# Kernel optimization log

Hardware: AMD Instinct MI355X
Metric: run time of the kernel (lower is better)

Reference implementation:

```python
import jax, jax.numpy as jnp
import numpy as np

N, D, NUM_CLASSES = 8192, 256, 64
MARGIN_SAME = 0.9
MARGIN_DIFF = 0.5


def setup_inputs() -> dict:
    key = jax.random.key(0)
    k1, k2 = jax.random.split(key)
    inputs = jax.random.normal(k1, (N, D), dtype=jnp.float32)
    # contrastive losses with cosine-style margins expect unit-norm embeddings
    inputs = inputs / jnp.linalg.norm(inputs, axis=1, keepdims=True)
    targets = jax.random.randint(k2, (N,), 0, NUM_CLASSES, dtype=jnp.int64)
    return {"inputs": inputs, "targets": targets}


def reference(inputs, targets):
    n = inputs.shape[0]
    sim = jnp.matmul(inputs, inputs.T)  # [n, n] pairwise similarities

    same = targets[:, None] == targets[None, :]  # [n, n]
    pos_mask = same & (sim < 1.0)                # pos_pair_ selection per row
    neg_mask = ~same                             # neg_pair_ selection per row

    pos_active = pos_mask & (sim < MARGIN_SAME)  # contribute 1 - sim
    neg_active = neg_mask & (sim > MARGIN_DIFF)  # contribute sim

    # sum over all rows, divided by n (sort in the original is irrelevant to sums)
    loss = (jnp.sum(jnp.where(pos_active, 1.0 - sim, 0.0))
            + jnp.sum(jnp.where(neg_active, sim, 0.0))) / n

    prec = jnp.float32(0.0)  # original: c is never incremented

    # original reports means of the LAST row's pos_pair_ / neg_pair_
    last_sim = sim[n - 1]
    lp = pos_mask[n - 1]
    ln = neg_mask[n - 1]
    mean_pos_sim = jnp.sum(jnp.where(lp, last_sim, 0.0)) / jnp.maximum(
        jnp.sum(lp).astype(jnp.float32), 1.0)
    mean_neg_sim = jnp.sum(jnp.where(ln, last_sim, 0.0)) / jnp.maximum(
        jnp.sum(ln).astype(jnp.float32), 1.0)

    return (loss, prec, mean_pos_sim, mean_neg_sim)
```

## Files before the change

### kernel.cpp

```cpp
#include <hip/hip_runtime.h>
#include <hip/hip_bf16.h>

#define N_ 8192
#define D_ 256
#define BM 128
#define NB (N_ / BM)
#define NT (NB * (NB + 1) / 2)

typedef float f32x4 __attribute__((ext_vector_type(4)));


__global__ void prep_kernel(const float* __restrict__ X, const int* __restrict__ tg,
                            unsigned char* __restrict__ Xb, double* __restrict__ accd) {
  if (blockIdx.x < 512) {
    if (blockIdx.x == 0 && threadIdx.x < 96) accd[threadIdx.x] = 0.0;
    int t = blockIdx.x * 256 + threadIdx.x;
    int r = t >> 4, pc = t & 15;
    int w = pc >> 2, s = pc & 3;
    const float* row = X + (size_t)r * D_;
    int ka = w * 64 + s * 8;
    float4 a0 = *(const float4*)(row + ka);
    float4 a1 = *(const float4*)(row + ka + 4);
    float4 b0 = *(const float4*)(row + ka + 32);
    float4 b1 = *(const float4*)(row + ka + 36);
    int4 d;
    d.x = __builtin_amdgcn_cvt_pk_fp8_f32(a0.x, a0.y, 0, false);
    d.x = __builtin_amdgcn_cvt_pk_fp8_f32(a0.z, a0.w, d.x, true);
    d.y = __builtin_amdgcn_cvt_pk_fp8_f32(a1.x, a1.y, 0, false);
    d.y = __builtin_amdgcn_cvt_pk_fp8_f32(a1.z, a1.w, d.y, true);
    d.z = __builtin_amdgcn_cvt_pk_fp8_f32(b0.x, b0.y, 0, false);
    d.z = __builtin_amdgcn_cvt_pk_fp8_f32(b0.z, b0.w, d.z, true);
    d.w = __builtin_amdgcn_cvt_pk_fp8_f32(b1.x, b1.y, 0, false);
    d.w = __builtin_amdgcn_cvt_pk_fp8_f32(b1.z, b1.w, d.w, true);
    *(int4*)(Xb + (size_t)r * 256 + pc * 16) = d;
  } else {
    int lb = blockIdx.x - 512;
    int lane = threadIdx.x & 63, wv = threadIdx.x >> 6;
    const float4* xl = (const float4*)(X + (size_t)(N_ - 1) * D_);
    float4 a = xl[lane];
    int tlast = tg[N_ - 1];
    double lp = 0, lpc = 0, ln = 0, lnc = 0;
    for (int cc = 0; cc < 16; ++cc) {
      int j = lb * 64 + wv * 16 + cc;
      float4 bq = ((const float4*)(X + (size_t)j * D_))[lane];
      double s = (double)a.x * bq.x + (double)a.y * bq.y +
                 (double)a.z * bq.z + (double)a.w * bq.w;
#pragma unroll
      for (int off = 32; off; off >>= 1) s += __shfl_down(s, off);
      if (lane == 0) {
        float sf = (float)s;
        bool same = (tg[j] == tlast);
        if (same && sf < 1.0f) { lp += sf; lpc += 1.0; }
        if (!same) { ln += sf; lnc += 1.0; }
      }
    }
    if (lane == 0) {
      double* slot = accd + 128 + (size_t)(lb * 4 + wv) * 4;
      slot[0] = lp; slot[1] = lpc; slot[2] = ln; slot[3] = lnc;
    }
  }
}

__global__ __launch_bounds__(256, 4) void simloss_kernel(
    const unsigned char* __restrict__ Xb, const int* __restrict__ tg,
    double* __restrict__ accd) {
  __shared__ __align__(16) char lds[2 * 16384];
  __shared__ float red[12];

  const int t0 = blockIdx.x;
  const int t = (t0 & 7) * (NT / 8) + (t0 >> 3);

  int bi = (int)(((2.0f * NB + 1.0f) -
                  sqrtf((2.0f * NB + 1.0f) * (2.0f * NB + 1.0f) - 8.0f * (float)t)) * 0.5f);
  if (bi < 0) bi = 0;
  if (bi > NB - 1) bi = NB - 1;
  while (((bi + 1) * NB - ((bi + 1) * bi) / 2) <= t) ++bi;
  while ((bi * NB - (bi * (bi - 1)) / 2) > t) --bi;
  const int bj = bi + (t - (bi * NB - (bi * (bi - 1)) / 2));

  const int tid = threadIdx.x;
  const int lane = tid & 63, wv = tid >> 6;
  const int wr = wv >> 1, wc = wv & 1;
  const int rowA0 = bi * BM, rowB0 = bj * BM;

  const int srow = tid >> 2;
  const int sw = (tid & 3) ^ ((srow >> 1) & 3);
  const unsigned char* bA = Xb + (size_t)(rowA0 + srow) * 256 + sw * 16;
  const unsigned char* bB = Xb + (size_t)(rowB0 + srow) * 256 + sw * 16;

#define GLDS(g, l) \
  __builtin_amdgcn_global_load_lds((const __attribute__((address_space(1))) void*)(g), \
                                   (__attribute__((address_space(3))) void*)(l), 16, 0, 0)
#define STAGE(buf, kt)                                       \
  do {                                                       \
    char* base = lds + (buf) * 16384;                        \
    GLDS(bA + (kt) * 64, base + tid * 16);                   \
    GLDS(bA + 16384 + (kt) * 64, base + 4096 + tid * 16);    \
    GLDS(bB + (kt) * 64, base + 8192 + tid * 16);            \
    GLDS(bB + 16384 + (kt) * 64, base + 12288 + tid * 16);   \
  } while (0)

  const int fr = lane & 15, slv = lane >> 4;
  const int rswz = slv ^ ((fr >> 1) & 3);
  const int aoff = (wr * 64 + fr) * 64 + rswz * 16;
  const int boff = 8192 + (wc * 64 + fr) * 64 + rswz * 16;

  f32x4 acc[4][4] = {};
  union U { int4 v; long l[2]; };

  STAGE(0, 0);
  STAGE(1, 1);

#pragma unroll
  for (int kt = 0; kt < 4; ++kt) {
    if (kt < 3)
      asm volatile("s_waitcnt vmcnt(4)" ::: "memory");
    else
      asm volatile("s_waitcnt vmcnt(0)" ::: "memory");
    __builtin_amdgcn_s_barrier();

    const char* Ab = lds + (kt & 1) * 16384;
    U a[4], b[4];
#pragma unroll
    for (int m = 0; m < 4; ++m) a[m].v = *(const int4*)(Ab + aoff + m * 1024);
#pragma unroll
    for (int n = 0; n < 4; ++n) b[n].v = *(const int4*)(Ab + boff + n * 1024);
#pragma unroll
    for (int m = 0; m < 4; ++m)
#pragma unroll
      for (int n = 0; n < 4; ++n) {
        acc[m][n] = __builtin_amdgcn_mfma_f32_16x16x32_fp8_fp8(a[m].l[0], b[n].l[0],
                                                               acc[m][n], 0, 0, 0);
        acc[m][n] = __builtin_amdgcn_mfma_f32_16x16x32_fp8_fp8(a[m].l[1], b[n].l[1],
                                                               acc[m][n], 0, 0, 0);
      }

    if (kt < 2) {
      asm volatile("s_waitcnt lgkmcnt(0)" ::: "memory");
      __builtin_amdgcn_sched_barrier(0);
      __builtin_amdgcn_s_barrier();
      STAGE(kt & 1, kt + 2);
    }
  }
#undef STAGE
#undef GLDS

  const int cRow = slv * 4, cCol = fr;
  int tj[4], ti[4][4];
#pragma unroll
  for (int n = 0; n < 4; ++n) tj[n] = tg[rowB0 + wc * 64 + n * 16 + cCol];
#pragma unroll
  for (int m = 0; m < 4; ++m)
#pragma unroll
    for (int r = 0; r < 4; ++r) ti[m][r] = tg[rowA0 + wr * 64 + m * 16 + cRow + r];

  float pc = 0.f, ps = 0.f, ns = 0.f;
#pragma unroll
  for (int m = 0; m < 4; ++m)
#pragma unroll
    for (int n = 0; n < 4; ++n)
#pragma unroll
      for (int r = 0; r < 4; ++r) {
        float s = acc[m][n][r];
        bool same = (ti[m][r] == tj[n]);
        if (same & (s < 0.9f)) { pc += 1.0f; ps += s; }
        if ((!same) & (s > 0.5f)) { ns += s; }
      }

#pragma unroll
  for (int off = 32; off > 0; off >>= 1) {
    pc += __shfl_down(pc, off);
    ps += __shfl_down(ps, off);
    ns += __shfl_down(ns, off);
  }
  if (lane == 0) { red[0 + wv] = pc; red[4 + wv] = ps; red[8 + wv] = ns; }
  __syncthreads();
  if (tid == 0) {
    double w = (bi == bj) ? 1.0 : 2.0;
    double* slot = accd + (blockIdx.x & 31) * 3;
    atomicAdd(&slot[0], w * (double)(red[0] + red[1] + red[2] + red[3]));
    atomicAdd(&slot[1], w * (double)(red[4] + red[5] + red[6] + red[7]));
    atomicAdd(&slot[2], w * (double)(red[8] + red[9] + red[10] + red[11]));
  }
}

__global__ void finalize_kernel(const double* __restrict__ accd, float* __restrict__ out) {
  int l = threadIdx.x;
  double lp = 0, lpc = 0, ln = 0, lnc = 0;
  for (int q = l; q < 512; q += 64) {
    const double* s = accd + 128 + (size_t)q * 4;
    lp += s[0]; lpc += s[1]; ln += s[2]; lnc += s[3];
  }
  double pc = 0, ps = 0, ns = 0;
  if (l < 32) { pc = accd[l * 3]; ps = accd[l * 3 + 1]; ns = accd[l * 3 + 2]; }
#pragma unroll
  for (int off = 32; off > 0; off >>= 1) {
    lp += __shfl_down(lp, off);  lpc += __shfl_down(lpc, off);
    ln += __shfl_down(ln, off);  lnc += __shfl_down(lnc, off);
    pc += __shfl_down(pc, off);  ps += __shfl_down(ps, off);
    ns += __shfl_down(ns, off);
  }
  if (l == 0) {
    out[0] = (float)((pc - ps + ns) / (double)N_);
    out[1] = 0.0f;
    out[2] = (float)(lp / fmax(lpc, 1.0));
    out[3] = (float)(ln / fmax(lnc, 1.0));
  }
}

extern "C" void kernel_launch(void* const* d_in, const int* in_sizes, int n_in,
                              void* d_out, int out_size, void* d_ws, size_t ws_size,
                              hipStream_t stream) {
  const float* X = (const float*)d_in[0];
  const int* tg = (const int*)d_in[1];
  float* out = (float*)d_out;
  double* accd = (double*)d_ws;
  unsigned char* Xb = (unsigned char*)d_ws + 32768;

  prep_kernel<<<512 + 128, 256, 0, stream>>>(X, tg, Xb, accd);
  simloss_kernel<<<NT, 256, 0, stream>>>(Xb, tg, accd);
  finalize_kernel<<<1, 64, 0, stream>>>(accd, out);
}
```

Measured before the change: 46.98 us.

## Process four column tiles per block reusing resident A tile in LDS

Each block now keeps its 128-row A tile resident in LDS for the full K depth and streams four consecutive B column tiles through a triple-buffered pipeline. Partial loss sums are reduced after each tile. The launch shrinks from 2080 single-tile blocks to 544 four-tile blocks, with padded tiles beyond the triangle given zero weight. This cuts redundant A loads and per-block overhead, but uses more LDS (launch bounds drop to 2) and wastes some work on padded tiles.

```diff
diff --git a/kernel.cpp b/kernel.cpp
--- a/kernel.cpp
+++ b/kernel.cpp
@@ -3,9 +3,7 @@
 
 #define N_ 8192
 #define D_ 256
-#define BM 128
-#define NB (N_ / BM)
-#define NT (NB * (NB + 1) / 2)
+#define NBLK 544
 
 typedef float f32x4 __attribute__((ext_vector_type(4)));
 
@@ -61,126 +59,158 @@
   }
 }
 
-__global__ __launch_bounds__(256, 4) void simloss_kernel(
+__global__ __launch_bounds__(256, 2) void simloss_kernel(
     const unsigned char* __restrict__ Xb, const int* __restrict__ tg,
     double* __restrict__ accd) {
-  __shared__ __align__(16) char lds[2 * 16384];
+  __shared__ __align__(16) char lds[32768 + 3 * 8192];
   __shared__ float red[12];
 
   const int t0 = blockIdx.x;
-  const int t = (t0 & 7) * (NT / 8) + (t0 >> 3);
-
-  int bi = (int)(((2.0f * NB + 1.0f) -
-                  sqrtf((2.0f * NB + 1.0f) * (2.0f * NB + 1.0f) - 8.0f * (float)t)) * 0.5f);
-  if (bi < 0) bi = 0;
-  if (bi > NB - 1) bi = NB - 1;
-  while (((bi + 1) * NB - ((bi + 1) * bi) / 2) <= t) ++bi;
-  while ((bi * NB - (bi * (bi - 1)) / 2) > t) --bi;
-  const int bj = bi + (t - (bi * NB - (bi * (bi - 1)) / 2));
+  const int b = (t0 & 7) * (NBLK / 8) + (t0 >> 3);
+#define FA(x) (66 * (x)-2 * (x) * (x))
+  int a = (int)((66.0f - sqrtf(4356.0f - 8.0f * (float)b)) * 0.25f);
+  if (a < 0) a = 0;
+  if (a > 15) a = 15;
+  while (a < 15 && FA(a + 1) <= b) ++a;
+  while (a > 0 && FA(a) > b) --a;
+  int off = b - FA(a);
+  const int nbb = 16 - a;
+  int r = 0;
+  while (off >= nbb) { off -= nbb; ++r; }
+  const int bi = 4 * a + r;
+  const int j0 = bi + 4 * off;
+#undef FA
 
   const int tid = threadIdx.x;
   const int lane = tid & 63, wv = tid >> 6;
   const int wr = wv >> 1, wc = wv & 1;
-  const int rowA0 = bi * BM, rowB0 = bj * BM;
+  const int rowA0 = bi * 128;
+
+  int bj[4];
+  float wt[4];
+#pragma unroll
+  for (int tt = 0; tt < 4; ++tt) {
+    int j = j0 + tt;
+    wt[tt] = (j > 63) ? 0.0f : (j == bi ? 1.0f : 2.0f);
+    bj[tt] = (j > 63) ? 63 : j;
+  }
+
+  const int fr = lane & 15, slv = lane >> 4;
+  const int cRow = slv * 4, cCol = fr;
+  int ti[4][4], tjq[4][4];
+#pragma unroll
+  for (int m = 0; m < 4; ++m) {
+    int4 v = *(const int4*)(tg + rowA0 + wr * 64 + m * 16 + cRow);
+    ti[m][0] = v.x; ti[m][1] = v.y; ti[m][2] = v.z; ti[m][3] = v.w;
+  }
+#pragma unroll
+  for (int tt = 0; tt < 4; ++tt)
+#pragma unroll
+    for (int n = 0; n < 4; ++n) tjq[tt][n] = tg[bj[tt] * 128 + wc * 64 + n * 16 + cCol];
 
   const int srow = tid >> 2;
   const int sw = (tid & 3) ^ ((srow >> 1) & 3);
   const unsigned char* bA = Xb + (size_t)(rowA0 + srow) * 256 + sw * 16;
-  const unsigned char* bB = Xb + (size_t)(rowB0 + srow) * 256 + sw * 16;
+  const unsigned char* pB[4];
+#pragma unroll
+  for (int tt = 0; tt < 4; ++tt)
+    pB[tt] = Xb + (size_t)(bj[tt] * 128 + srow) * 256 + sw * 16;
 
 #define GLDS(g, l) \
   __builtin_amdgcn_global_load_lds((const __attribute__((address_space(1))) void*)(g), \
                                    (__attribute__((address_space(3))) void*)(l), 16, 0, 0)
-#define STAGE(buf, kt)                                       \
-  do {                                                       \
-    char* base = lds + (buf) * 16384;                        \
-    GLDS(bA + (kt) * 64, base + tid * 16);                   \
-    GLDS(bA + 16384 + (kt) * 64, base + 4096 + tid * 16);    \
-    GLDS(bB + (kt) * 64, base + 8192 + tid * 16);            \
-    GLDS(bB + 16384 + (kt) * 64, base + 12288 + tid * 16);   \
+#define STAGE_B(s)                                              \
+  do {                                                          \
+    char* d = lds + 32768 + ((s) % 3) * 8192;                   \
+    const unsigned char* src = pB[(s) >> 2] + ((s)&3) * 64;     \
+    GLDS(src, d + tid * 16);                                    \
+    GLDS(src + 16384, d + 4096 + tid * 16);                     \
   } while (0)
 
-  const int fr = lane & 15, slv = lane >> 4;
+  __builtin_amdgcn_sched_barrier(0);
+#pragma unroll
+  for (int kt = 0; kt < 4; ++kt) {
+    GLDS(bA + kt * 64, lds + kt * 8192 + tid * 16);
+    GLDS(bA + 16384 + kt * 64, lds + kt * 8192 + 4096 + tid * 16);
+  }
+  STAGE_B(0);
+  STAGE_B(1);
+
   const int rswz = slv ^ ((fr >> 1) & 3);
   const int aoff = (wr * 64 + fr) * 64 + rswz * 16;
-  const int boff = 8192 + (wc * 64 + fr) * 64 + rswz * 16;
+  const int boff = (wc * 64 + fr) * 64 + rswz * 16;
 
   f32x4 acc[4][4] = {};
+  float pcT = 0.f, psT = 0.f, nsT = 0.f;
   union U { int4 v; long l[2]; };
 
-  STAGE(0, 0);
-  STAGE(1, 1);
-
-#pragma unroll
-  for (int kt = 0; kt < 4; ++kt) {
-    if (kt < 3)
-      asm volatile("s_waitcnt vmcnt(4)" ::: "memory");
+#pragma unroll
+  for (int s = 0; s < 16; ++s) {
+    asm volatile("s_waitcnt lgkmcnt(0)" ::: "memory");
+    __builtin_amdgcn_sched_barrier(0);
+    if (s < 15)
+      asm volatile("s_waitcnt vmcnt(2)" ::: "memory");
     else
       asm volatile("s_waitcnt vmcnt(0)" ::: "memory");
     __builtin_amdgcn_s_barrier();
-
-    const char* Ab = lds + (kt & 1) * 16384;
-    U a[4], b[4];
-#pragma unroll
-    for (int m = 0; m < 4; ++m) a[m].v = *(const int4*)(Ab + aoff + m * 1024);
-#pragma unroll
-    for (int n = 0; n < 4; ++n) b[n].v = *(const int4*)(Ab + boff + n * 1024);
+    if (s + 2 < 16) STAGE_B(s + 2);
+
+    const int kt = s & 3, tt = s >> 2;
+    const char* Ab = lds + kt * 8192;
+    const char* Bb = lds + 32768 + (s % 3) * 8192;
+    U a4[4], b4[4];
+#pragma unroll
+    for (int m = 0; m < 4; ++m) a4[m].v = *(const int4*)(Ab + aoff + m * 1024);
+#pragma unroll
+    for (int n = 0; n < 4; ++n) b4[n].v = *(const int4*)(Bb + boff + n * 1024);
 #pragma unroll
     for (int m = 0; m < 4; ++m)
 #pragma unroll
       for (int n = 0; n < 4; ++n) {
-        acc[m][n] = __builtin_amdgcn_mfma_f32_16x16x32_fp8_fp8(a[m].l[0], b[n].l[0],
+        acc[m][n] = __builtin_amdgcn_mfma_f32_16x16x32_fp8_fp8(a4[m].l[0], b4[n].l[0],
                                                                acc[m][n], 0, 0, 0);
-        acc[m][n] = __builtin_amdgcn_mfma_f32_16x16x32_fp8_fp8(a[m].l[1], b[n].l[1],
+        acc[m][n] = __builtin_amdgcn_mfma_f32_16x16x32_fp8_fp8(a4[m].l[1], b4[n].l[1],
                                                                acc[m][n], 0, 0, 0);
       }
 
-    if (kt < 2) {
-      asm volatile("s_waitcnt lgkmcnt(0)" ::: "memory");
-      __builtin_amdgcn_sched_barrier(0);
-      __builtin_amdgcn_s_barrier();
-      STAGE(kt & 1, kt + 2);
+    if (kt == 3) {
+      float pc = 0.f, ps = 0.f, ns = 0.f;
+#pragma unroll
+      for (int m = 0; m < 4; ++m)
+#pragma unroll
+        for (int n = 0; n < 4; ++n)
+#pragma unroll
+          for (int rg = 0; rg < 4; ++rg) {
+            float sv = acc[m][n][rg];
+            bool same = (ti[m][rg] == tjq[tt][n]);
+            if (same & (sv < 0.9f)) { pc += 1.0f; ps += sv; }
+            if ((!same) & (sv > 0.5f)) { ns += sv; }
+          }
+      pcT += wt[tt] * pc;
+      psT += wt[tt] * ps;
+      nsT += wt[tt] * ns;
+#pragma unroll
+      for (int m = 0; m < 4; ++m)
+#pragma unroll
+        for (int n = 0; n < 4; ++n) acc[m][n] = f32x4{0.f, 0.f, 0.f, 0.f};
     }
   }
-#undef STAGE
+#undef STAGE_B
 #undef GLDS
 
-  const int cRow = slv * 4, cCol = fr;
-  int tj[4], ti[4][4];
-#pragma unroll
-  for (int n = 0; n < 4; ++n) tj[n] = tg[rowB0 + wc * 64 + n * 16 + cCol];
-#pragma unroll
-  for (int m = 0; m < 4; ++m)
-#pragma unroll
-    for (int r = 0; r < 4; ++r) ti[m][r] = tg[rowA0 + wr * 64 + m * 16 + cRow + r];
-
-  float pc = 0.f, ps = 0.f, ns = 0.f;
-#pragma unroll
-  for (int m = 0; m < 4; ++m)
-#pragma unroll
-    for (int n = 0; n < 4; ++n)
-#pragma unroll
-      for (int r = 0; r < 4; ++r) {
-        float s = acc[m][n][r];
-        bool same = (ti[m][r] == tj[n]);
-        if (same & (s < 0.9f)) { pc += 1.0f; ps += s; }
-        if ((!same) & (s > 0.5f)) { ns += s; }
-      }
-
-#pragma unroll
-  for (int off = 32; off > 0; off >>= 1) {
-    pc += __shfl_down(pc, off);
-    ps += __shfl_down(ps, off);
-    ns += __shfl_down(ns, off);
-  }
-  if (lane == 0) { red[0 + wv] = pc; red[4 + wv] = ps; red[8 + wv] = ns; }
+#pragma unroll
+  for (int off2 = 32; off2 > 0; off2 >>= 1) {
+    pcT += __shfl_down(pcT, off2);
+    psT += __shfl_down(psT, off2);
+    nsT += __shfl_down(nsT, off2);
+  }
+  if (lane == 0) { red[0 + wv] = pcT; red[4 + wv] = psT; red[8 + wv] = nsT; }
   __syncthreads();
   if (tid == 0) {
-    double w = (bi == bj) ? 1.0 : 2.0;
     double* slot = accd + (blockIdx.x & 31) * 3;
-    atomicAdd(&slot[0], w * (double)(red[0] + red[1] + red[2] + red[3]));
-    atomicAdd(&slot[1], w * (double)(red[4] + red[5] + red[6] + red[7]));
-    atomicAdd(&slot[2], w * (double)(red[8] + red[9] + red[10] + red[11]));
+    atomicAdd(&slot[0], (double)(red[0] + red[1] + red[2] + red[3]));
+    atomicAdd(&slot[1], (double)(red[4] + red[5] + red[6] + red[7]));
+    atomicAdd(&slot[2], (double)(red[8] + red[9] + red[10] + red[11]));
   }
 }
 
@@ -218,6 +248,6 @@
   unsigned char* Xb = (unsigned char*)d_ws + 32768;
 
   prep_kernel<<<512 + 128, 256, 0, stream>>>(X, tg, Xb, accd);
-  simloss_kernel<<<NT, 256, 0, stream>>>(Xb, tg, accd);
+  simloss_kernel<<<NBLK, 256, 0, stream>>>(Xb, tg, accd);
   finalize_kernel<<<1, 64, 0, stream>>>(accd, out);
 }
```

Result: slower. 55.79 us (+18.7%).
